# Optimization experiments

Hardware: AMD Instinct MI355X
Metric: run time of the kernel (lower is better)

## Reference

```python
import jax, jax.numpy as jnp
import numpy as np

BN_EPS = 1e-5


def conv1d(x, w, stride, pad):
    # x: [N, C, T], w: [O, I, K]
    return jax.lax.conv_general_dilated(
        x, w, window_strides=(stride,), padding=[(pad, pad)],
        dimension_numbers=('NCH', 'OIH', 'NCH'))


def setup_inputs() -> dict:
    key = jax.random.key(0)
    ks = jax.random.split(key, 10)
    B, Cin, T = 32, 80, 1024
    C, D, M = 768, 64, 512
    s = 0.02
    inp = {
        'mels': jax.random.normal(ks[0], (B, Cin, T), jnp.float32),
        'w1': jax.random.normal(ks[1], (C, Cin, 3), jnp.float32) * s,
        'w2': jax.random.normal(ks[2], (C, C, 3), jnp.float32) * s,
        'w3': jax.random.normal(ks[3], (C, C, 4), jnp.float32) * s,
        'w4': jax.random.normal(ks[4], (C, C, 3), jnp.float32) * s,
        'w5': jax.random.normal(ks[5], (C, C, 3), jnp.float32) * s,
        'w6': jax.random.normal(ks[6], (D, C, 1), jnp.float32) * s,
        'b6': jnp.zeros((D,), jnp.float32),
        'bn_gamma': jnp.ones((5, C), jnp.float32),
        'bn_beta': jnp.zeros((5, C), jnp.float32),
        'bn_mean': jnp.zeros((5, C), jnp.float32),
        'bn_var': jnp.ones((5, C), jnp.float32),
        'embedding': jax.random.uniform(ks[7], (M, D), jnp.float32,
                                        minval=-1.0 / 512, maxval=1.0 / 512),
    }
    return inp


def reference(mels, w1, w2, w3, w4, w5, w6, b6,
              bn_gamma, bn_beta, bn_mean, bn_var, embedding):
    def block(x, w, stride, pad, i):
        x = conv1d(x, w, stride, pad)
        inv = bn_gamma[i] / jnp.sqrt(bn_var[i] + BN_EPS)
        x = x * inv[None, :, None] + (bn_beta[i] - bn_mean[i] * inv)[None, :, None]
        return jax.nn.relu(x)

    z = block(mels, w1, 1, 0, 0)   # [B, C, 1022]
    z = block(z, w2, 1, 1, 1)
    z = block(z, w3, 2, 1, 2)      # [B, C, 511]
    z = block(z, w4, 1, 1, 3)
    z = block(z, w5, 1, 1, 4)
    z = conv1d(z, w6, 1, 0) + b6[None, :, None]  # [B, D, 511]
    z = jnp.transpose(z, (0, 2, 1))              # [B, T', D]

    B, Tp, D = z.shape
    M = embedding.shape[0]
    x_flat = jax.lax.stop_gradient(z).reshape(-1, D)  # [N, D]
    dists = (jnp.sum(embedding ** 2, axis=1)[None, :]
             + jnp.sum(x_flat ** 2, axis=1, keepdims=True)
             - 2.0 * x_flat @ embedding.T)
    idx = jnp.argmin(dists, axis=-1)                  # [N]
    quantized = embedding[idx].reshape(B, Tp, D)
    loss = 0.25 * jnp.mean((z - jax.lax.stop_gradient(quantized)) ** 2)
    q_st = z + jax.lax.stop_gradient(quantized - z)   # straight-through
    counts = jnp.zeros((M,), jnp.float32).at[idx].add(1.0)
    avg_probs = counts / idx.shape[0]
    perplexity = jnp.exp(-jnp.sum(avg_probs * jnp.log(avg_probs + 1e-10)))
    return (q_st, loss, perplexity)
```

## Files before the change

### kernel.cpp

```cpp
#include <hip/hip_runtime.h>
#include <cstddef>
#include <cstdint>

#define BN_EPS 1e-5f

typedef _Float16 half8 __attribute__((ext_vector_type(8)));
typedef float f32x4v __attribute__((ext_vector_type(4)));

__device__ __forceinline__ unsigned split_pack(float v) {
    _Float16 h = (_Float16)v;
    float r = (v - (float)h) * 2048.0f;
    _Float16 l = (_Float16)r;
    unsigned short hu = __builtin_bit_cast(unsigned short, h);
    unsigned short lu = __builtin_bit_cast(unsigned short, l);
    return (unsigned)hu | ((unsigned)lu << 16);
}

__device__ __forceinline__ void splitHL(uint4 a, uint4 b2, uint4& h, uint4& l) {
    h.x = (a.x & 0xffffu) | (a.y << 16);
    h.y = (a.z & 0xffffu) | (a.w << 16);
    h.z = (b2.x & 0xffffu) | (b2.y << 16);
    h.w = (b2.z & 0xffffu) | (b2.w << 16);
    l.x = (a.x >> 16) | (a.y & 0xffff0000u);
    l.y = (a.z >> 16) | (a.w & 0xffff0000u);
    l.z = (b2.x >> 16) | (b2.y & 0xffff0000u);
    l.w = (b2.z >> 16) | (b2.w & 0xffff0000u);
}

__global__ __launch_bounds__(256)
void prep_w(const float* __restrict__ w, unsigned short* __restrict__ wh,
            unsigned short* __restrict__ wl, int Cin, int KW, int CIPAD)
{
    int id = blockIdx.x * 256 + threadIdx.x;
    int total = KW * 768 * CIPAD;
    if (id >= total) return;
    int cip = id % CIPAD;
    int co  = (id / CIPAD) % 768;
    int kw  = id / (CIPAD * 768);
    float v = 0.0f;
    if (cip < Cin) v = w[((size_t)co * Cin + cip) * KW + kw];
    unsigned pk = split_pack(v * 256.0f);
    wh[id] = (unsigned short)pk;
    wl[id] = (unsigned short)(pk >> 16);
}

__global__ __launch_bounds__(256)
void prep_mels(const float* __restrict__ mels, unsigned short* __restrict__ mh,
               unsigned short* __restrict__ ml)
{
    int id = blockIdx.x * 256 + threadIdx.x;
    if (id >= 32 * 1032 * 96) return;
    int c = id % 96;
    int t = (id / 96) % 1032;
    int b = id / (96 * 1032);
    float v = 0.0f;
    if (c < 80 && t < 1024) v = mels[((size_t)b * 80 + c) * 1024 + t];
    unsigned pk = split_pack(v * 16.0f);
    mh[id] = (unsigned short)pk;
    ml[id] = (unsigned short)(pk >> 16);
}

template<int KW, int S, int P, int CIPAD, int TIN, int TSIN, int TOUT, int TSOUT, int EPI>
__global__ __launch_bounds__(512, 4)
void conv_mfma(const unsigned short* __restrict__ XH, const unsigned short* __restrict__ XL,
               const unsigned short* __restrict__ WH, const unsigned short* __restrict__ WL,
               const float* __restrict__ gamma, const float* __restrict__ beta,
               const float* __restrict__ mean, const float* __restrict__ var,
               unsigned short* __restrict__ OutH, unsigned short* __restrict__ OutL,
               float* __restrict__ Fout)
{
    constexpr int NCI = CIPAD / 32;
    constexpr int NC  = KW * NCI;
    __shared__ unsigned smem[16896];
    _Float16* sm = (_Float16*)smem;

    const int gx = gridDim.x, gy = gridDim.y;
    const int nwg  = gx * gy * (int)gridDim.z;
    const int flat = blockIdx.x + gx * (blockIdx.y + gy * blockIdx.z);
    const int swz  = (flat & 7) * (nwg >> 3) + (flat >> 3);
    const int cox  = swz % gx;
    const int rem  = swz / gx;
    const int ty   = rem % gy;
    const int b    = rem / gy;

    const int co0 = cox * 128;
    const int t0  = ty * 128;
    const int tid = threadIdx.x;
    const int lane = tid & 63, wv = tid >> 6;
    const int quad = lane >> 4, l16 = lane & 15;
    const int wm = (wv & 1) * 64;
    const int wn = (wv >> 1) * 32;

    f32x4v accH[4][2] = {};
    f32x4v accX[4][2] = {};

    const int ab   = tid >> 8;
    const int r2   = tid & 255;
    const int srow = r2 >> 1;
    const int sh   = r2 & 1;
    const unsigned short* __restrict__ xhb = XH + (size_t)b * TSIN * CIPAD;
    const unsigned short* __restrict__ xlb = XL + (size_t)b * TSIN * CIPAD;

    uint4 rH[2], rL[2];

    auto loadT = [&](int c) {
        const int kw  = c / NCI;
        const int ci0 = (c % NCI) * 32;
        if (ab == 0) {
            const size_t o = (size_t)(kw * 768 + co0 + srow) * CIPAD + ci0;
            rH[0] = *(const uint4*)(WH + o + sh * 8);
            rH[1] = *(const uint4*)(WH + o + (sh + 2) * 8);
            rL[0] = *(const uint4*)(WL + o + sh * 8);
            rL[1] = *(const uint4*)(WL + o + (sh + 2) * 8);
        } else {
            const int tp = (t0 + srow) * S + kw - P;
            rH[0] = rH[1] = rL[0] = rL[1] = make_uint4(0, 0, 0, 0);
            if ((unsigned)tp < (unsigned)TIN) {
                const size_t o = (size_t)tp * CIPAD + ci0;
                rH[0] = *(const uint4*)(xhb + o + sh * 8);
                rH[1] = *(const uint4*)(xhb + o + (sh + 2) * 8);
                rL[0] = *(const uint4*)(xlb + o + sh * 8);
                rL[1] = *(const uint4*)(xlb + o + (sh + 2) * 8);
            }
        }
    };

    auto storeT = [&](int pbuf) {
        const int b0 = pbuf * 16384 + ab * 8192;
        const int u1 = (((srow >> 4) * 4 + sh) * 16 + (srow & 15)) * 8;
        const int u2 = u1 + 256;
        *(uint4*)(sm + b0 + 0    + u1) = rH[0];
        *(uint4*)(sm + b0 + 4096 + u1) = rL[0];
        *(uint4*)(sm + b0 + 0    + u2) = rH[1];
        *(uint4*)(sm + b0 + 4096 + u2) = rL[1];
    };

    loadT(0);
    storeT(0);
    if (NC > 1) loadT(1);
    __syncthreads();

    int p = 0;
    for (int c = 0; c < NC; ++c) {
        const int base = p * 16384;
        if (c + 1 < NC) storeT(p ^ 1);
        if (c + 2 < NC) loadT(c + 2);

        half8 bh[2], bl[2];
#pragma unroll
        for (int nt = 0; nt < 2; ++nt) {
            int gn = (wv >> 1) * 2 + nt;
            int u = ((gn * 4 + quad) * 16 + l16) * 8;
            bh[nt] = *(const half8*)(sm + base + 8192  + u);
            bl[nt] = *(const half8*)(sm + base + 12288 + u);
        }
#pragma unroll
        for (int mt = 0; mt < 4; ++mt) {
            int gm = (wv & 1) * 4 + mt;
            int u = ((gm * 4 + quad) * 16 + l16) * 8;
            half8 ah = *(const half8*)(sm + base + 0    + u);
            half8 al = *(const half8*)(sm + base + 4096 + u);
#pragma unroll
            for (int nt = 0; nt < 2; ++nt) {
                accH[mt][nt] = __builtin_amdgcn_mfma_f32_16x16x32_f16(ah, bh[nt], accH[mt][nt], 0, 0, 0);
                accX[mt][nt] = __builtin_amdgcn_mfma_f32_16x16x32_f16(ah, bl[nt], accX[mt][nt], 0, 0, 0);
                accX[mt][nt] = __builtin_amdgcn_mfma_f32_16x16x32_f16(al, bh[nt], accX[mt][nt], 0, 0, 0);
            }
        }
        __syncthreads();
        p ^= 1;
    }

    if constexpr (EPI == 0) {
        unsigned* bb = smem;
#pragma unroll
        for (int mt = 0; mt < 4; ++mt) {
#pragma unroll
            for (int r = 0; r < 4; ++r) {
                int mloc = wm + mt * 16 + quad * 4 + r;
                int co = co0 + mloc;
                float iv = gamma[co] / sqrtf(var[co] + BN_EPS);
                float sh2 = beta[co] - mean[co] * iv;
#pragma unroll
                for (int nt = 0; nt < 2; ++nt) {
                    float vf = (accH[mt][nt][r] + accX[mt][nt][r] * (1.0f / 2048.0f)) * (1.0f / 4096.0f);
                    float y = fmaf(vf, iv, sh2);
                    y = y > 0.0f ? y : 0.0f;
                    bb[(wn + nt * 16 + l16) * 132 + mloc] = split_pack(y * 16.0f);
                }
            }
        }
        __syncthreads();
        int tl = tid >> 2, seg = tid & 3;
        int t = t0 + tl;
        if (t < TOUT) {
            const uint4* src = (const uint4*)(bb + tl * 132 + seg * 32);
            size_t base2 = ((size_t)b * TSOUT + t) * 768 + co0 + seg * 32;
#pragma unroll
            for (int i = 0; i < 4; ++i) {
                uint4 h, l;
                splitHL(src[2 * i], src[2 * i + 1], h, l);
                *(uint4*)(OutH + base2 + i * 8) = h;
                *(uint4*)(OutL + base2 + i * 8) = l;
            }
        }
    } else {
#pragma unroll
        for (int mt = 0; mt < 4; ++mt) {
#pragma unroll
            for (int r = 0; r < 4; ++r) {
                int co = co0 + wm + mt * 16 + quad * 4 + r;
                float iv = gamma[co] / sqrtf(var[co] + BN_EPS);
                float sh2 = beta[co] - mean[co] * iv;
                float* op = Fout + ((size_t)b * 768 + co) * TOUT;
#pragma unroll
                for (int nt = 0; nt < 2; ++nt) {
                    int t = t0 + wn + nt * 16 + l16;
                    if (t < TOUT) {
                        float vf = (accH[mt][nt][r] + accX[mt][nt][r] * (1.0f / 2048.0f)) * (1.0f / 4096.0f);
                        float y = fmaf(vf, iv, sh2);
                        op[t] = y > 0.0f ? y : 0.0f;
                    }
                }
            }
        }
    }
}

constexpr int TM = 64, TN = 64, TK = 16;

__global__ __launch_bounds__(256)
void conv1x1_bias_T(const float* __restrict__ in, const float* __restrict__ w,
                    const float* __restrict__ bias, float* __restrict__ z,
                    int Cin, int T)
{
    const int b   = blockIdx.z;
    const int t0  = blockIdx.y * TN;
    const int tid = threadIdx.x;

    __shared__ float As[TK][TM + 4];
    __shared__ float Bs[TK][TN + 4];

    float acc[4][4] = {};

    const int m0 = (tid & 15) * 4;
    const int n0 = (tid >> 4) * 4;

    const float* __restrict__ inb = in + (size_t)b * Cin * T;

    const int a_m = tid >> 4;
    const int a_k = tid & 15;
    const int b_k = tid >> 6;
    const int b_n = tid & 63;

    for (int kc = 0; kc < Cin; kc += TK) {
        __syncthreads();
#pragma unroll
        for (int i = 0; i < 4; ++i) {
            int m = a_m + 16 * i;
            As[a_k][m] = w[(size_t)m * Cin + kc + a_k];
        }
#pragma unroll
        for (int i = 0; i < 4; ++i) {
            int kk = b_k + 4 * i;
            int ci = kc + kk;
            int t  = t0 + b_n;
            Bs[kk][b_n] = (t < T) ? inb[(size_t)ci * T + t] : 0.0f;
        }
        __syncthreads();
#pragma unroll
        for (int kk = 0; kk < TK; ++kk) {
            float4 av = *reinterpret_cast<const float4*>(&As[kk][m0]);
            float4 bv = *reinterpret_cast<const float4*>(&Bs[kk][n0]);
            float am[4] = {av.x, av.y, av.z, av.w};
            float bn[4] = {bv.x, bv.y, bv.z, bv.w};
#pragma unroll
            for (int mi = 0; mi < 4; ++mi)
#pragma unroll
                for (int nj = 0; nj < 4; ++nj)
                    acc[mi][nj] = fmaf(am[mi], bn[nj], acc[mi][nj]);
        }
    }

    float4 bb = *reinterpret_cast<const float4*>(&bias[m0]);
    float bs[4] = {bb.x, bb.y, bb.z, bb.w};
#pragma unroll
    for (int nj = 0; nj < 4; ++nj) {
        int t = t0 + n0 + nj;
        if (t < T) {
            float4 v;
            v.x = acc[0][nj] + bs[0];
            v.y = acc[1][nj] + bs[1];
            v.z = acc[2][nj] + bs[2];
            v.w = acc[3][nj] + bs[3];
            *reinterpret_cast<float4*>(&z[((size_t)b * T + t) * 64 + m0]) = v;
        }
    }
}

__global__ __launch_bounds__(256)
void vq_e2(const float* __restrict__ emb, float* __restrict__ e2)
{
    int m = blockIdx.x * 256 + threadIdx.x;
    if (m < 512) {
        float s = 0.0f;
#pragma unroll
        for (int d = 0; d < 64; ++d) {
            float v = emb[(size_t)m * 64 + d];
            s = fmaf(v, v, s);
        }
        e2[m] = s;
    }
}

__global__ __launch_bounds__(64)
void vq_argmin(const float* __restrict__ z, const float* __restrict__ emb,
               const float* __restrict__ e2, int* __restrict__ idx,
               float* __restrict__ counts, int N)
{
    __shared__ float Es[64 * 64];
    const int tid = threadIdx.x;
    const int n   = blockIdx.x * 64 + tid;
    const bool act = n < N;

    float x[64];
    float x2 = 0.0f;
    if (act) {
        const float4* zp = reinterpret_cast<const float4*>(z + (size_t)n * 64);
#pragma unroll
        for (int i = 0; i < 16; ++i) {
            float4 v = zp[i];
            x[4 * i + 0] = v.x; x[4 * i + 1] = v.y;
            x[4 * i + 2] = v.z; x[4 * i + 3] = v.w;
        }
#pragma unroll
        for (int d = 0; d < 64; ++d) x2 = fmaf(x[d], x[d], x2);
    }

    float best = 3.4e38f;
    int   bi   = 0;
    for (int c = 0; c < 8; ++c) {
        __syncthreads();
        const float4* ep  = reinterpret_cast<const float4*>(emb + (size_t)c * 4096);
        float4*       esp = reinterpret_cast<float4*>(Es);
#pragma unroll
        for (int i = 0; i < 16; ++i) esp[tid + 64 * i] = ep[tid + 64 * i];
        __syncthreads();
        for (int r = 0; r < 64; ++r) {
            const float4* er = reinterpret_cast<const float4*>(&Es[r * 64]);
            float dot = 0.0f;
#pragma unroll
            for (int i = 0; i < 16; ++i) {
                float4 e4 = er[i];
                dot = fmaf(x[4 * i + 0], e4.x, dot);
                dot = fmaf(x[4 * i + 1], e4.y, dot);
                dot = fmaf(x[4 * i + 2], e4.z, dot);
                dot = fmaf(x[4 * i + 3], e4.w, dot);
            }
            float dist = (e2[c * 64 + r] + x2) - 2.0f * dot;
            if (dist < best) { best = dist; bi = c * 64 + r; }
        }
    }
    if (act) {
        idx[n] = bi;
        atomicAdd(&counts[bi], 1.0f);
    }
}

__global__ __launch_bounds__(256)
void vq_quant_loss(const float* __restrict__ z, const float* __restrict__ emb,
                   const int* __restrict__ idx, float* __restrict__ qout,
                   double* __restrict__ loss_sum, int Ntot)
{
    int g = blockIdx.x * 256 + threadIdx.x;
    float d2 = 0.0f;
    if (g < Ntot) {
        int n = g >> 6;
        int d = g & 63;
        float q  = emb[(size_t)idx[n] * 64 + d];
        float zv = z[g];
        qout[g] = zv + (q - zv);
        float diff = zv - q;
        d2 = diff * diff;
    }
#pragma unroll
    for (int o = 32; o > 0; o >>= 1) d2 += __shfl_down(d2, o);
    __shared__ float wsum[4];
    if ((threadIdx.x & 63) == 0) wsum[threadIdx.x >> 6] = d2;
    __syncthreads();
    if (threadIdx.x == 0)
        atomicAdd(loss_sum, (double)(wsum[0] + wsum[1] + wsum[2] + wsum[3]));
}

__global__ __launch_bounds__(512)
void vq_finalize(const float* __restrict__ counts, const double* __restrict__ loss_sum,
                 float* __restrict__ out, int Ntot, int Npts)
{
    int t = threadIdx.x;
    float c   = counts[t];
    float avg = c / (float)Npts;
    float term = avg * logf(avg + 1e-10f);
#pragma unroll
    for (int o = 32; o > 0; o >>= 1) term += __shfl_down(term, o);
    __shared__ float wsum[8];
    if ((t & 63) == 0) wsum[t >> 6] = term;
    __syncthreads();
    if (t == 0) {
        float s = 0.0f;
        for (int i = 0; i < 8; ++i) s += wsum[i];
        out[Ntot]     = 0.25f * (float)(loss_sum[0] / (double)Ntot);
        out[Ntot + 1] = expf(-s);
    }
}

extern "C" void kernel_launch(void* const* d_in, const int* in_sizes, int n_in,
                              void* d_out, int out_size, void* d_ws, size_t ws_size,
                              hipStream_t stream)
{
    const float* mels     = (const float*)d_in[0];
    const float* w1       = (const float*)d_in[1];
    const float* w2       = (const float*)d_in[2];
    const float* w3       = (const float*)d_in[3];
    const float* w4       = (const float*)d_in[4];
    const float* w5       = (const float*)d_in[5];
    const float* w6       = (const float*)d_in[6];
    const float* b6       = (const float*)d_in[7];
    const float* bn_gamma = (const float*)d_in[8];
    const float* bn_beta  = (const float*)d_in[9];
    const float* bn_mean  = (const float*)d_in[10];
    const float* bn_var   = (const float*)d_in[11];
    const float* emb      = (const float*)d_in[12];

    constexpr int B = 32, C = 768, D = 64, T2 = 511;

    char* ws = (char*)d_ws;
    constexpr size_t ACT = (size_t)32 * 1024 * 768;
    unsigned short* P1H = (unsigned short*)ws;
    unsigned short* P1L = P1H + ACT;
    unsigned short* P2H = (unsigned short*)(ws + 100663296);
    unsigned short* P2L = P2H + ACT;
    unsigned short* WHp = (unsigned short*)(ws + 201326592);
    unsigned short* WLp = WHp + (size_t)4 * 768 * 768;
    size_t misc  = 201326592 + 9437184;
    float*  counts = (float*)(ws + misc);
    double* lossp  = (double*)(ws + misc + 2048);
    float*  e2p    = (float*)(ws + misc + 2048 + 64);
    int*    idx    = (int*)(ws + misc + 2048 + 64 + 2048);

    unsigned short* MH = P2H;
    unsigned short* ML = P2L;
    float* bufA = (float*)ws;
    float* z    = (float*)(ws + 100663296);

    hipMemsetAsync(ws + misc, 0, 2048 + 64, stream);

    vq_e2<<<dim3(2), 256, 0, stream>>>(emb, e2p);
    prep_mels<<<dim3((32 * 1032 * 96 + 255) / 256), 256, 0, stream>>>(mels, MH, ML);

    prep_w<<<dim3((3 * 768 * 96 + 255) / 256), 256, 0, stream>>>(w1, WHp, WLp, 80, 3, 96);
    conv_mfma<3, 1, 0, 96, 1032, 1032, 1022, 1024, 0><<<dim3(6, 8, B), 512, 0, stream>>>(
        MH, ML, WHp, WLp, bn_gamma + 0 * C, bn_beta + 0 * C, bn_mean + 0 * C, bn_var + 0 * C,
        P1H, P1L, nullptr);
    prep_w<<<dim3((3 * 768 * 768 + 255) / 256), 256, 0, stream>>>(w2, WHp, WLp, 768, 3, 768);
    conv_mfma<3, 1, 1, 768, 1022, 1024, 1022, 1024, 0><<<dim3(6, 8, B), 512, 0, stream>>>(
        P1H, P1L, WHp, WLp, bn_gamma + 1 * C, bn_beta + 1 * C, bn_mean + 1 * C, bn_var + 1 * C,
        P2H, P2L, nullptr);
    prep_w<<<dim3((4 * 768 * 768 + 255) / 256), 256, 0, stream>>>(w3, WHp, WLp, 768, 4, 768);
    conv_mfma<4, 2, 1, 768, 1022, 1024, 511, 512, 0><<<dim3(6, 4, B), 512, 0, stream>>>(
        P2H, P2L, WHp, WLp, bn_gamma + 2 * C, bn_beta + 2 * C, bn_mean + 2 * C, bn_var + 2 * C,
        P1H, P1L, nullptr);
    prep_w<<<dim3((3 * 768 * 768 + 255) / 256), 256, 0, stream>>>(w4, WHp, WLp, 768, 3, 768);
    conv_mfma<3, 1, 1, 768, 511, 512, 511, 512, 0><<<dim3(6, 4, B), 512, 0, stream>>>(
        P1H, P1L, WHp, WLp, bn_gamma + 3 * C, bn_beta + 3 * C, bn_mean + 3 * C, bn_var + 3 * C,
        P2H, P2L, nullptr);
    prep_w<<<dim3((3 * 768 * 768 + 255) / 256), 256, 0, stream>>>(w5, WHp, WLp, 768, 3, 768);
    conv_mfma<3, 1, 1, 768, 511, 512, 511, 511, 1><<<dim3(6, 4, B), 512, 0, stream>>>(
        P2H, P2L, WHp, WLp, bn_gamma + 4 * C, bn_beta + 4 * C, bn_mean + 4 * C, bn_var + 4 * C,
        nullptr, nullptr, bufA);

    conv1x1_bias_T<<<dim3(1, 8, B), 256, 0, stream>>>(bufA, w6, b6, z, C, T2);

    const int Npts = B * T2;
    const int Ntot = Npts * D;
    vq_argmin<<<dim3((Npts + 63) / 64), 64, 0, stream>>>(z, emb, e2p, idx, counts, Npts);
    vq_quant_loss<<<dim3(Ntot / 256), 256, 0, stream>>>(z, emb, idx, (float*)d_out, lossp, Ntot);
    vq_finalize<<<dim3(1), 512, 0, stream>>>(counts, lossp, (float*)d_out, Ntot, Npts);
}
```

Measured before the change: 1.483 ms.

## Split VQ argmin codebook across four waves and use lighter LDS barrier in conv

The VQ argmin kernel now runs 256 threads per block. Each of four waves scans a quarter of the 512-entry codebook for the same 64 points, and the per-wave minima are reduced through shared memory with an index tie-break. This raises parallelism for a kernel that previously had one wave per block. The conv MFMA loop replaces __syncthreads with an explicit lgkmcnt wait plus s_barrier, which avoids waiting on outstanding global prefetch loads (vmcnt) at each barrier. That barrier relies on LDS stores being covered by lgkmcnt alone, and the argmin kernel now uses a 64KB LDS tile.

New measurement: 1.394 ms, median of 2. 6.0% less time.

```diff
diff --git a/kernel.cpp b/kernel.cpp
--- a/kernel.cpp
+++ b/kernel.cpp
@@ -135,10 +135,16 @@
         *(uint4*)(sm + b0 + 4096 + u2) = rL[1];
     };
 
+    auto ldsBarrier = [] {
+        asm volatile("s_waitcnt lgkmcnt(0)" ::: "memory");
+        __builtin_amdgcn_s_barrier();
+        asm volatile("" ::: "memory");
+    };
+
     loadT(0);
     storeT(0);
     if (NC > 1) loadT(1);
-    __syncthreads();
+    ldsBarrier();
 
     int p = 0;
     for (int c = 0; c < NC; ++c) {
@@ -167,7 +173,7 @@
                 accX[mt][nt] = __builtin_amdgcn_mfma_f32_16x16x32_f16(al, bh[nt], accX[mt][nt], 0, 0, 0);
             }
         }
-        __syncthreads();
+        ldsBarrier();
         p ^= 1;
     }
 
@@ -313,14 +319,18 @@
     }
 }
 
-__global__ __launch_bounds__(64)
+__global__ __launch_bounds__(256)
 void vq_argmin(const float* __restrict__ z, const float* __restrict__ emb,
                const float* __restrict__ e2, int* __restrict__ idx,
                float* __restrict__ counts, int N)
 {
-    __shared__ float Es[64 * 64];
+    __shared__ float Es[256 * 64];
+    __shared__ float bestS[4][64];
+    __shared__ int   biS[4][64];
     const int tid = threadIdx.x;
-    const int n   = blockIdx.x * 64 + tid;
+    const int pt  = tid & 63;
+    const int wvq = tid >> 6;
+    const int n   = blockIdx.x * 64 + pt;
     const bool act = n < N;
 
     float x[64];
@@ -339,15 +349,16 @@
 
     float best = 3.4e38f;
     int   bi   = 0;
-    for (int c = 0; c < 8; ++c) {
+    for (int pass = 0; pass < 2; ++pass) {
         __syncthreads();
-        const float4* ep  = reinterpret_cast<const float4*>(emb + (size_t)c * 4096);
+        const float4* ep  = reinterpret_cast<const float4*>(emb + (size_t)pass * 16384);
         float4*       esp = reinterpret_cast<float4*>(Es);
 #pragma unroll
-        for (int i = 0; i < 16; ++i) esp[tid + 64 * i] = ep[tid + 64 * i];
+        for (int i = 0; i < 16; ++i) esp[tid + 256 * i] = ep[tid + 256 * i];
         __syncthreads();
+        const int c = pass * 4 + wvq;
         for (int r = 0; r < 64; ++r) {
-            const float4* er = reinterpret_cast<const float4*>(&Es[r * 64]);
+            const float4* er = reinterpret_cast<const float4*>(&Es[((size_t)wvq * 64 + r) * 64]);
             float dot = 0.0f;
 #pragma unroll
             for (int i = 0; i < 16; ++i) {
@@ -361,9 +372,20 @@
             if (dist < best) { best = dist; bi = c * 64 + r; }
         }
     }
-    if (act) {
-        idx[n] = bi;
-        atomicAdd(&counts[bi], 1.0f);
+    bestS[wvq][pt] = best;
+    biS[wvq][pt]   = bi;
+    __syncthreads();
+    if (wvq == 0 && act) {
+        float bd = bestS[0][pt];
+        int   bx = biS[0][pt];
+#pragma unroll
+        for (int g = 1; g < 4; ++g) {
+            float d = bestS[g][pt];
+            int   i2 = biS[g][pt];
+            if (d < bd || (d == bd && i2 < bx)) { bd = d; bx = i2; }
+        }
+        idx[n] = bx;
+        atomicAdd(&counts[bx], 1.0f);
     }
 }
 
@@ -482,7 +504,7 @@
 
     const int Npts = B * T2;
     const int Ntot = Npts * D;
-    vq_argmin<<<dim3((Npts + 63) / 64), 64, 0, stream>>>(z, emb, e2p, idx, counts, Npts);
+    vq_argmin<<<dim3((Npts + 63) / 64), 256, 0, stream>>>(z, emb, e2p, idx, counts, Npts);
     vq_quant_loss<<<dim3(Ntot / 256), 256, 0, stream>>>(z, emb, idx, (float*)d_out, lossp, Ntot);
     vq_finalize<<<dim3(1), 512, 0, stream>>>(counts, lossp, (float*)d_out, Ntot, Npts);
 }
```
